# Performance work log

Hardware: AMD Instinct MI355X
Metric: run time of the kernel (lower is better)

## Reference

```python
import jax, jax.numpy as jnp
import numpy as np

EMBED = 256
MAX_NL = 2
NP = 9
NH = 1


def bilinear_sample(img, grid):
    # img: [C, H, W]; grid: [N, 2] (x, y) in [-1, 1]
    # F.grid_sample(mode='bilinear', padding_mode='zeros', align_corners=False)
    C, H, W = img.shape
    x = (grid[:, 0] + 1.0) * (W * 0.5) - 0.5
    y = (grid[:, 1] + 1.0) * (H * 0.5) - 0.5
    x0 = jnp.floor(x)
    y0 = jnp.floor(y)
    wx1 = x - x0
    wy1 = y - y0
    img_f = img.reshape(C, H * W)

    def corner(xi, yi, w):
        valid = (xi >= 0) & (xi <= W - 1) & (yi >= 0) & (yi <= H - 1)
        idx = (jnp.clip(yi, 0, H - 1).astype(jnp.int32) * W
               + jnp.clip(xi, 0, W - 1).astype(jnp.int32))
        return img_f[:, idx] * (w * valid)[None, :]

    return (corner(x0, y0, (1 - wx1) * (1 - wy1))
            + corner(x0 + 1, y0, wx1 * (1 - wy1))
            + corner(x0, y0 + 1, (1 - wx1) * wy1)
            + corner(x0 + 1, y0 + 1, wx1 * wy1))  # [C, N]


def setup_inputs() -> dict:
    k = jax.random.key(0)
    ks = jax.random.split(k, 5)
    nq = 20000
    H = W = 128
    nv = H * W
    nl = 2
    C = EMBED
    query = jax.random.normal(ks[0], (1, nq, C), jnp.float32)
    key = jnp.zeros((1, nq, C), jnp.float32)  # unused by forward
    value = jax.random.normal(ks[1], (nl, nv, C), jnp.float32)
    reference_points = jax.random.uniform(ks[2], (1, nq, nl, 2), jnp.float32)
    spatial_shapes = jnp.array([[H, W], [H, W]], jnp.int32)
    W_off = jax.random.normal(ks[3], (C, MAX_NL * NH * NP * 2), jnp.float32) * 0.02
    b_off = jax.random.normal(ks[4], (MAX_NL * NH * NP * 2,), jnp.float32) * 0.02
    return {"query": query, "key": key, "value": value,
            "reference_points": reference_points, "spatial_shapes": spatial_shapes,
            "W_off": W_off, "b_off": b_off}


def reference(query, key, value, reference_points, spatial_shapes, W_off, b_off):
    nl, nv, C = value.shape
    bs, nq, _ = query.shape
    # sampling offsets: [bs, nq, NH, max_nl, NP, 2], sliced to nl levels
    off = (query @ W_off + b_off).reshape(bs, nq, NH, MAX_NL, NP, 2)[:, :, :, :nl]
    # normalizer stacks (W, H) per level
    norm = jnp.stack([spatial_shapes[:, 1], spatial_shapes[:, 0]], -1).astype(query.dtype)
    loc = reference_points[:, :, None, :, None, :] + off / norm[None, None, None, :, None, :]
    grids = 2.0 * loc - 1.0  # [1, nq, 1, nl, NP, 2]
    sampled = []
    for l in range(nl):
        H = int(spatial_shapes[l, 0]); W = int(spatial_shapes[l, 1])
        img = value[l].T.reshape(C, H, W)
        g = grids[0, :, 0, l, :, :].reshape(nq * NP, 2)
        sampled.append(bilinear_sample(img, g).reshape(C, nq, NP))
    # stack levels then flatten points: [1, nq, nl*NP, C]
    kv = jnp.stack(sampled, axis=-2).reshape(C, nq, nl * NP).transpose(1, 2, 0)[None]
    # note: original multiplies by sqrt(dim) (not divide) -- kept faithful
    attn = jax.nn.softmax(jnp.einsum('bqc,bqpc->bqp', query, kv)
                          * jnp.sqrt(jnp.float32(C)), axis=-1)
    return jnp.einsum('bqp,bqpc->bqc', attn, kv)
```

## Files before the change

### kernel.cpp

```cpp
#include <hip/hip_runtime.h>

#define C_EMB 256
#define NPL   9
#define NLV   2
#define NPTS  (NPL * NLV)
#define NJ    (NPTS * 2)

__global__ void transpose_woff(const float* __restrict__ W_off, float* __restrict__ WT) {
    int j = blockIdx.x;
    int c = threadIdx.x;
    WT[j * C_EMB + c] = W_off[c * NJ + j];
}

__device__ __forceinline__ int imin(int a, int b) { return a < b ? a : b; }
__device__ __forceinline__ int imax(int a, int b) { return a > b ? a : b; }

template<int CTRL, int ROW_MASK>
__device__ __forceinline__ float dpp_add(float x) {
    int t = __builtin_amdgcn_update_dpp(0, __builtin_bit_cast(int, x),
                                        CTRL, ROW_MASK, 0xf, true);
    return x + __builtin_bit_cast(float, t);
}

__device__ __forceinline__ float wave_sum_all(float x) {
    x = dpp_add<0x111, 0xf>(x);
    x = dpp_add<0x112, 0xf>(x);
    x = dpp_add<0x114, 0xf>(x);
    x = dpp_add<0x118, 0xf>(x);
    x = dpp_add<0x142, 0xa>(x);
    x = dpp_add<0x143, 0xc>(x);
    int r = __builtin_amdgcn_readlane(__builtin_bit_cast(int, x), 63);
    return __builtin_bit_cast(float, r);
}

template<bool USE_WT>
__global__ __launch_bounds__(256)
void deform_attn_kernel(const float* __restrict__ query,
                        const float* __restrict__ value,
                        const float* __restrict__ refp,
                        const int*   __restrict__ sshapes,
                        const float* __restrict__ WT,
                        const float* __restrict__ W_off,
                        const float* __restrict__ b_off,
                        float*       __restrict__ out,
                        int nq, int nv) {
    const int lane = threadIdx.x & 63;
    const int widx = threadIdx.x >> 6;
    const int q = blockIdx.x * 4 + widx;
    if (q >= nq) return;

    __shared__ int4   s_idx[4][NPTS];
    __shared__ float4 s_w[4][NPTS];

    const float4 q4 = *reinterpret_cast<const float4*>(query + (size_t)q * C_EMB + lane * 4);

    float ox = 0.f, oy = 0.f;
    #pragma unroll
    for (int j = 0; j < NJ; ++j) {
        float s;
        if (USE_WT) {
            float4 w4 = *reinterpret_cast<const float4*>(WT + j * C_EMB + lane * 4);
            s = q4.x * w4.x + q4.y * w4.y + q4.z * w4.z + q4.w * w4.w;
        } else {
            const float* wp = W_off + (lane * 4) * NJ + j;
            s = q4.x * wp[0] + q4.y * wp[NJ] + q4.z * wp[2 * NJ] + q4.w * wp[3 * NJ];
        }
        s = wave_sum_all(s) + b_off[j];
        if (j == 2 * lane)     ox = s;
        if (j == 2 * lane + 1) oy = s;
    }

    if (lane < NPTS) {
        int l = lane / NPL;
        int Hi = sshapes[l * 2 + 0];
        int Wi = sshapes[l * 2 + 1];
        float fw = (float)Wi, fh = (float)Hi;
        float rx = refp[((size_t)q * NLV + l) * 2 + 0];
        float ry = refp[((size_t)q * NLV + l) * 2 + 1];
        float x = rx * fw + ox - 0.5f;
        float y = ry * fh + oy - 0.5f;
        float x0f = floorf(x), y0f = floorf(y);
        int x0 = (int)x0f, y0 = (int)y0f;
        float wx1 = x - x0f, wy1 = y - y0f;
        float wx0 = 1.f - wx1, wy0 = 1.f - wy1;
        bool vx0 = (x0 >= 0) && (x0 <= Wi - 1);
        bool vx1 = (x0 + 1 >= 0) && (x0 + 1 <= Wi - 1);
        bool vy0 = (y0 >= 0) && (y0 <= Hi - 1);
        bool vy1 = (y0 + 1 >= 0) && (y0 + 1 <= Hi - 1);
        int cx0 = imin(imax(x0, 0), Wi - 1);
        int cx1 = imin(imax(x0 + 1, 0), Wi - 1);
        int cy0 = imin(imax(y0, 0), Hi - 1);
        int cy1 = imin(imax(y0 + 1, 0), Hi - 1);
        int base = l * nv;
        int4 id;
        id.x = base + cy0 * Wi + cx0;
        id.y = base + cy0 * Wi + cx1;
        id.z = base + cy1 * Wi + cx0;
        id.w = base + cy1 * Wi + cx1;
        float4 w;
        w.x = wx0 * wy0 * ((vx0 && vy0) ? 1.f : 0.f);
        w.y = wx1 * wy0 * ((vx1 && vy0) ? 1.f : 0.f);
        w.z = wx0 * wy1 * ((vx0 && vy1) ? 1.f : 0.f);
        w.w = wx1 * wy1 * ((vx1 && vy1) ? 1.f : 0.f);
        s_idx[widx][lane] = id;
        s_w[widx][lane]   = w;
    }
    __builtin_amdgcn_wave_barrier();

    const int coff = lane * 4;
    float4 kv[NPTS];
    float  lg[NPTS];
    #pragma unroll
    for (int p = 0; p < NPTS; ++p) {
        int4   id = s_idx[widx][p];
        float4 w  = s_w[widx][p];
        const float4 a = *reinterpret_cast<const float4*>(value + (size_t)id.x * C_EMB + coff);
        const float4 b = *reinterpret_cast<const float4*>(value + (size_t)id.y * C_EMB + coff);
        const float4 c = *reinterpret_cast<const float4*>(value + (size_t)id.z * C_EMB + coff);
        const float4 d = *reinterpret_cast<const float4*>(value + (size_t)id.w * C_EMB + coff);
        float4 acc;
        acc.x = w.x * a.x + w.y * b.x + w.z * c.x + w.w * d.x;
        acc.y = w.x * a.y + w.y * b.y + w.z * c.y + w.w * d.y;
        acc.z = w.x * a.z + w.y * b.z + w.z * c.z + w.w * d.z;
        acc.w = w.x * a.w + w.y * b.w + w.z * c.w + w.w * d.w;
        kv[p] = acc;
        lg[p] = q4.x * acc.x + q4.y * acc.y + q4.z * acc.z + q4.w * acc.w;
    }

    #pragma unroll
    for (int p = 0; p < NPTS; ++p) {
        lg[p] = wave_sum_all(lg[p]) * 16.0f;
    }

    float m = lg[0];
    #pragma unroll
    for (int p = 1; p < NPTS; ++p) m = fmaxf(m, lg[p]);
    float sum = 0.f;
    #pragma unroll
    for (int p = 0; p < NPTS; ++p) { lg[p] = __expf(lg[p] - m); sum += lg[p]; }
    float inv = 1.0f / sum;

    float4 o; o.x = 0.f; o.y = 0.f; o.z = 0.f; o.w = 0.f;
    #pragma unroll
    for (int p = 0; p < NPTS; ++p) {
        o.x += lg[p] * kv[p].x;
        o.y += lg[p] * kv[p].y;
        o.z += lg[p] * kv[p].z;
        o.w += lg[p] * kv[p].w;
    }
    o.x *= inv; o.y *= inv; o.z *= inv; o.w *= inv;
    *reinterpret_cast<float4*>(out + (size_t)q * C_EMB + coff) = o;
}

extern "C" void kernel_launch(void* const* d_in, const int* in_sizes, int n_in,
                              void* d_out, int out_size, void* d_ws, size_t ws_size,
                              hipStream_t stream) {
    const float* query = (const float*)d_in[0];
    const float* value = (const float*)d_in[2];
    const float* refp  = (const float*)d_in[3];
    const int*   ss    = (const int*)d_in[4];
    const float* W_off = (const float*)d_in[5];
    const float* b_off = (const float*)d_in[6];
    float* out = (float*)d_out;

    const int nq = in_sizes[0] / C_EMB;
    const int nl = in_sizes[4] / 2;
    const int nv = in_sizes[2] / (nl * C_EMB);

    const int blocks = (nq + 3) / 4;

    const size_t wt_bytes = (size_t)NJ * C_EMB * sizeof(float);
    if (ws_size >= wt_bytes) {
        float* WT = (float*)d_ws;
        transpose_woff<<<NJ, C_EMB, 0, stream>>>(W_off, WT);
        deform_attn_kernel<true><<<blocks, 256, 0, stream>>>(
            query, value, refp, ss, WT, W_off, b_off, out, nq, nv);
    } else {
        deform_attn_kernel<false><<<blocks, 256, 0, stream>>>(
            query, value, refp, ss, nullptr, W_off, b_off, out, nq, nv);
    }
}
```

Baseline: 84.37 us.

## Split offset projection into separate kernel and use one-wave blocks

Moves the query·W_off offset projection out of the attention kernel into its own kernel. That kernel assigns one output column per lane, writes the offsets to workspace, and drops the 36 wave-wide DPP reductions per query. The main kernel now runs one 64-thread block per query and reads precomputed offsets. The trade is an extra launch, a second read of the query rows, and a workspace round trip, with many more small blocks in the main kernel.

Measured after the change: 146.4 us. 1.74x slower.

```diff
diff --git a/kernel.cpp b/kernel.cpp
--- a/kernel.cpp
+++ b/kernel.cpp
@@ -5,12 +5,6 @@
 #define NLV   2
 #define NPTS  (NPL * NLV)
 #define NJ    (NPTS * 2)
-
-__global__ void transpose_woff(const float* __restrict__ W_off, float* __restrict__ WT) {
-    int j = blockIdx.x;
-    int c = threadIdx.x;
-    WT[j * C_EMB + c] = W_off[c * NJ + j];
-}
 
 __device__ __forceinline__ int imin(int a, int b) { return a < b ? a : b; }
 __device__ __forceinline__ int imax(int a, int b) { return a > b ? a : b; }
@@ -33,41 +27,62 @@
     return __builtin_bit_cast(float, r);
 }
 
-template<bool USE_WT>
 __global__ __launch_bounds__(256)
+void offsets_kernel(const float* __restrict__ query,
+                    const float* __restrict__ W_off,
+                    const float* __restrict__ b_off,
+                    float* __restrict__ off_out, int nq) {
+    const int lane = threadIdx.x & 63;
+    const int widx = threadIdx.x >> 6;
+    const int q = blockIdx.x * 4 + widx;
+    if (q >= nq) return;
+    const float* qrow = query + (size_t)q * C_EMB;
+    const int j = (lane < NJ) ? lane : (NJ - 1);
+    float a0 = 0.f, a1 = 0.f;
+    #pragma unroll 8
+    for (int c = 0; c < C_EMB; c += 2) {
+        a0 = fmaf(qrow[c],     W_off[(c)     * NJ + j], a0);
+        a1 = fmaf(qrow[c + 1], W_off[(c + 1) * NJ + j], a1);
+    }
+    if (lane < NJ) off_out[(size_t)q * NJ + j] = a0 + a1 + b_off[j];
+}
+
+template<bool PRE>
+__global__ __launch_bounds__(64)
 void deform_attn_kernel(const float* __restrict__ query,
                         const float* __restrict__ value,
                         const float* __restrict__ refp,
                         const int*   __restrict__ sshapes,
-                        const float* __restrict__ WT,
+                        const float* __restrict__ off_pre,
                         const float* __restrict__ W_off,
                         const float* __restrict__ b_off,
                         float*       __restrict__ out,
                         int nq, int nv) {
-    const int lane = threadIdx.x & 63;
-    const int widx = threadIdx.x >> 6;
-    const int q = blockIdx.x * 4 + widx;
+    const int lane = threadIdx.x;
+    const int q = blockIdx.x;
     if (q >= nq) return;
 
-    __shared__ int4   s_idx[4][NPTS];
-    __shared__ float4 s_w[4][NPTS];
+    __shared__ int4   s_idx[NPTS];
+    __shared__ float4 s_w[NPTS];
 
-    const float4 q4 = *reinterpret_cast<const float4*>(query + (size_t)q * C_EMB + lane * 4);
+    const int coff = lane * 4;
+    const float4 q4 = *reinterpret_cast<const float4*>(query + (size_t)q * C_EMB + coff);
 
     float ox = 0.f, oy = 0.f;
-    #pragma unroll
-    for (int j = 0; j < NJ; ++j) {
-        float s;
-        if (USE_WT) {
-            float4 w4 = *reinterpret_cast<const float4*>(WT + j * C_EMB + lane * 4);
-            s = q4.x * w4.x + q4.y * w4.y + q4.z * w4.z + q4.w * w4.w;
-        } else {
+    if (PRE) {
+        if (lane < NPTS) {
+            float2 o2 = *reinterpret_cast<const float2*>(off_pre + (size_t)q * NJ + 2 * lane);
+            ox = o2.x; oy = o2.y;
+        }
+    } else {
+        #pragma unroll
+        for (int j = 0; j < NJ; ++j) {
             const float* wp = W_off + (lane * 4) * NJ + j;
-            s = q4.x * wp[0] + q4.y * wp[NJ] + q4.z * wp[2 * NJ] + q4.w * wp[3 * NJ];
+            float s = q4.x * wp[0] + q4.y * wp[NJ] + q4.z * wp[2 * NJ] + q4.w * wp[3 * NJ];
+            s = wave_sum_all(s) + b_off[j];
+            if (j == 2 * lane)     ox = s;
+            if (j == 2 * lane + 1) oy = s;
         }
-        s = wave_sum_all(s) + b_off[j];
-        if (j == 2 * lane)     ox = s;
-        if (j == 2 * lane + 1) oy = s;
     }
 
     if (lane < NPTS) {
@@ -102,18 +117,17 @@
         w.y = wx1 * wy0 * ((vx1 && vy0) ? 1.f : 0.f);
         w.z = wx0 * wy1 * ((vx0 && vy1) ? 1.f : 0.f);
         w.w = wx1 * wy1 * ((vx1 && vy1) ? 1.f : 0.f);
-        s_idx[widx][lane] = id;
-        s_w[widx][lane]   = w;
+        s_idx[lane] = id;
+        s_w[lane]   = w;
     }
     __builtin_amdgcn_wave_barrier();
 
-    const int coff = lane * 4;
     float4 kv[NPTS];
     float  lg[NPTS];
     #pragma unroll
     for (int p = 0; p < NPTS; ++p) {
-        int4   id = s_idx[widx][p];
-        float4 w  = s_w[widx][p];
+        int4   id = s_idx[p];
+        float4 w  = s_w[p];
         const float4 a = *reinterpret_cast<const float4*>(value + (size_t)id.x * C_EMB + coff);
         const float4 b = *reinterpret_cast<const float4*>(value + (size_t)id.y * C_EMB + coff);
         const float4 c = *reinterpret_cast<const float4*>(value + (size_t)id.z * C_EMB + coff);
@@ -167,16 +181,14 @@
     const int nl = in_sizes[4] / 2;
     const int nv = in_sizes[2] / (nl * C_EMB);
 
-    const int blocks = (nq + 3) / 4;
-
-    const size_t wt_bytes = (size_t)NJ * C_EMB * sizeof(float);
-    if (ws_size >= wt_bytes) {
-        float* WT = (float*)d_ws;
-        transpose_woff<<<NJ, C_EMB, 0, stream>>>(W_off, WT);
-        deform_attn_kernel<true><<<blocks, 256, 0, stream>>>(
-            query, value, refp, ss, WT, W_off, b_off, out, nq, nv);
+    const size_t off_bytes = (size_t)nq * NJ * sizeof(float);
+    if (ws_size >= off_bytes) {
+        float* off_ws = (float*)d_ws;
+        offsets_kernel<<<(nq + 3) / 4, 256, 0, stream>>>(query, W_off, b_off, off_ws, nq);
+        deform_attn_kernel<true><<<nq, 64, 0, stream>>>(
+            query, value, refp, ss, off_ws, W_off, b_off, out, nq, nv);
     } else {
-        deform_attn_kernel<false><<<blocks, 256, 0, stream>>>(
+        deform_attn_kernel<false><<<nq, 64, 0, stream>>>(
             query, value, refp, ss, nullptr, W_off, b_off, out, nq, nv);
     }
 }
```
